# Performance work log

Measured on AMD Instinct MI355X. Metric: run time of the kernel, lower is better.

Reference implementation:

```python
import jax, jax.numpy as jnp
import numpy as np

CAUSAL = True


def setup_inputs() -> dict:
    key = jax.random.key(0)
    k1, k2, k3 = jax.random.split(key, 3)
    B, H, T, D = 2, 16, 2048, 64
    q = jax.random.normal(k1, (B, H, T, D), dtype=jnp.float32)
    k = jax.random.normal(k2, (B, H, T, D), dtype=jnp.float32)
    v = jax.random.normal(k3, (B, H, T, D), dtype=jnp.float32)
    return {"q": q, "k": k, "v": v}


def reference(q, k, v):
    # q,k,v: [B,H,T,D]
    d = q.shape[-1]
    scale = d ** -0.5
    dots = jnp.einsum('bhid,bhjd->bhij', q, k) * scale  # [B,H,T,T]
    if CAUSAL:
        t = q.shape[2]
        mask = jnp.triu(jnp.ones((t, t), dtype=bool), k=1)  # True above diagonal
        dots = jnp.where(mask, -jnp.inf, dots)
    attn = jax.nn.softmax(dots, axis=-1)
    # torch.einsum('bhjd,bhij->bhid', v, attn) == attn @ v
    return jnp.einsum('bhij,bhjd->bhid', attn, v)
```

## Files before the change

### kernel.cpp

```cpp
#include <hip/hip_runtime.h>
#include <hip/hip_bf16.h>

typedef unsigned short u16;
typedef unsigned int u32;
typedef __bf16 bf16x8 __attribute__((ext_vector_type(8)));
typedef u16 u16x8 __attribute__((ext_vector_type(8)));
typedef float floatx4 __attribute__((ext_vector_type(4)));

#define T_SEQ 2048
#define HDIM 64
#define NBH 32

static __device__ __forceinline__ u16 f2b_rne(float x) {
    union { float f; u32 u; } c; c.f = x;
    u32 u = c.u;
    return (u16)((u + 0x7fffu + ((u >> 16) & 1u)) >> 16);
}
static __device__ __forceinline__ u16 f2b_trunc(float x) {
    union { float f; u32 u; } c; c.f = x;
    return (u16)(c.u >> 16);
}

#define GLOAD_LDS16(gp, lp)                                                      \
    __builtin_amdgcn_global_load_lds(                                            \
        (const __attribute__((address_space(1))) u32*)(gp),                      \
        (__attribute__((address_space(3))) u32*)(lp), 16, 0, 0)

#define WAIT_VM(N) asm volatile("s_waitcnt vmcnt(" #N ")" ::: "memory")

__global__ __launch_bounds__(256) void prep(const float* __restrict__ k,
                                            const float* __restrict__ v,
                                            u16* __restrict__ kb,
                                            u16* __restrict__ vt) {
    __shared__ u16 tile[64][68];
    const int bh = blockIdx.y, t0 = blockIdx.x * 64;
    const int tid = threadIdx.x;

    const float* ksrc = k + ((size_t)bh * T_SEQ + t0) * HDIM;
    u16* kdst = kb + ((size_t)bh * T_SEQ + t0) * HDIM;
#pragma unroll
    for (int p = 0; p < 4; p++) {
        int idx = p * 256 + tid;
        float4 f = ((const float4*)ksrc)[idx];
        ushort4 o;
        o.x = f2b_rne(f.x); o.y = f2b_rne(f.y); o.z = f2b_rne(f.z); o.w = f2b_rne(f.w);
        ((ushort4*)kdst)[idx] = o;
    }

    const float* vsrc = v + ((size_t)bh * T_SEQ + t0) * HDIM;
#pragma unroll
    for (int p = 0; p < 4; p++) {
        int idx = p * 256 + tid;
        int r = idx >> 4, c4 = (idx & 15) * 4;
        float4 f = *(const float4*)(vsrc + r * HDIM + c4);
        tile[c4 + 0][r] = f2b_rne(f.x);
        tile[c4 + 1][r] = f2b_rne(f.y);
        tile[c4 + 2][r] = f2b_rne(f.z);
        tile[c4 + 3][r] = f2b_rne(f.w);
    }
    __syncthreads();
    u16* dst = vt + (size_t)bh * HDIM * T_SEQ + t0;
#pragma unroll
    for (int p = 0; p < 2; p++) {
        int idx = p * 256 + tid;
        int d = idx >> 3, pb = idx & 7;
        int k0 = (pb >> 2) * 32 + (pb & 3) * 4;
        union { u16x8 v8; ushort4 q[2]; } w;
        w.q[0] = *(ushort4*)&tile[d][k0];
        w.q[1] = *(ushort4*)&tile[d][k0 + 16];
        *(u16x8*)(dst + (size_t)d * T_SEQ + pb * 8) = w.v8;
    }
}

__global__ __launch_bounds__(512, 4) void fattn(const float* __restrict__ q,
                                                const u16* __restrict__ kb,
                                                const u16* __restrict__ vtb,
                                                float* __restrict__ out) {
    __shared__ __align__(16) u16 Kl[4][64 * 64];
    __shared__ __align__(16) u16 Vl[4][64 * 64];

    const int id = blockIdx.x;
    const int xcd = id & 7;
    const int u = id >> 3;
    const int bh = xcd * 4 + (u & 3);
    const int s = u >> 2;
    const int pr = (s & 8) ? (s ^ 7) : s;
    const int qtHi = 31 - pr, qtLo = pr;

    const int tid = threadIdx.x;
    const int wave = tid >> 6, lane = tid & 63;
    const int l15 = lane & 15, quad = lane >> 4;
    const int tile_sel = wave >> 2;
    const int qhalf = (wave >> 1) & 1;
    const int khalf = wave & 1;
    const int qt = tile_sel ? qtLo : qtHi;
    const int qrow_base = qt * 64 + qhalf * 32;

    const float* qp = q + (size_t)bh * T_SEQ * HDIM;
    const u16* kp = kb + (size_t)bh * T_SEQ * HDIM;
    const u16* vp = vtb + (size_t)bh * HDIM * T_SEQ;

    const int srow = wave * 8 + (lane >> 3);
    const int slot = lane & 7;
    const u16* kg0 = kp + srow * HDIM + (slot ^ (srow & 7)) * 8;
    const u16* vg0 = vp + (size_t)srow * T_SEQ + ((slot - srow) & 7) * 8;

    auto stage = [&](int j, int buf) {
        GLOAD_LDS16(kg0 + j * 64 * HDIM, &Kl[buf][wave * 512]);
        GLOAD_LDS16(vg0 + j * 64, &Vl[buf][wave * 512]);
    };

    const float SL2E = 0.125f * 1.44269504088896f;
    bf16x8 qf[2][2];
    {
#pragma unroll
        for (int qb = 0; qb < 2; qb++) {
            const float* qrow = qp + (size_t)(qrow_base + qb * 16 + l15) * HDIM;
#pragma unroll
            for (int kc = 0; kc < 2; kc++) {
                const float4* p4 = (const float4*)(qrow + kc * 32 + quad * 8);
                float4 fa = p4[0], fb = p4[1];
                union { bf16x8 v; u16 s[8]; } cv;
                cv.s[0] = f2b_rne(fa.x * SL2E); cv.s[1] = f2b_rne(fa.y * SL2E);
                cv.s[2] = f2b_rne(fa.z * SL2E); cv.s[3] = f2b_rne(fa.w * SL2E);
                cv.s[4] = f2b_rne(fb.x * SL2E); cv.s[5] = f2b_rne(fb.y * SL2E);
                cv.s[6] = f2b_rne(fb.z * SL2E); cv.s[7] = f2b_rne(fb.w * SL2E);
                qf[qb][kc] = cv.v;
            }
        }
    }

    union { u16 h[8]; bf16x8 v; } onesu;
#pragma unroll
    for (int i = 0; i < 8; i++) onesu.h[i] = 0x3F80;
    const bf16x8 ones = onesu.v;

    stage(0, 0);
    stage(1, 1);
    stage(2, 2);

    floatx4 o_acc[2][4];
    floatx4 lsacc[2];
#pragma unroll
    for (int qb = 0; qb < 2; qb++) {
        lsacc[qb] = (floatx4){0.f, 0.f, 0.f, 0.f};
#pragma unroll
        for (int dt = 0; dt < 4; dt++) o_acc[qb][dt] = (floatx4){0.f, 0.f, 0.f, 0.f};
    }

    for (int j = 0; j <= qtHi; ++j) {
        if (j + 2 <= qtHi)      WAIT_VM(4);
        else if (j + 1 <= qtHi) WAIT_VM(2);
        else                    WAIT_VM(0);
        __builtin_amdgcn_s_barrier();

        const int cur = j & 3;
        const bool active = (j <= qt);

        bf16x8 kf[2][2];
        if (active) {
            const u16* Kc = Kl[cur];
#pragma unroll
            for (int kc = 0; kc < 2; kc++)
#pragma unroll
                for (int kb2 = 0; kb2 < 2; kb2++) {
                    int rk = khalf * 32 + kb2 * 16 + l15;
                    kf[kc][kb2] = *(const bf16x8*)(Kc + rk * 64 + ((kc * 4 + quad) ^ (rk & 7)) * 8);
                }
        }
        if (j + 3 <= qtHi) stage(j + 3, (j + 3) & 3);
        if (!active) continue;

        floatx4 sacc[2][2];
#pragma unroll
        for (int kb2 = 0; kb2 < 2; kb2++)
#pragma unroll
            for (int qb = 0; qb < 2; qb++) sacc[kb2][qb] = (floatx4){0.f, 0.f, 0.f, 0.f};
        __builtin_amdgcn_s_setprio(1);
#pragma unroll
        for (int kc = 0; kc < 2; kc++)
#pragma unroll
            for (int kb2 = 0; kb2 < 2; kb2++)
#pragma unroll
                for (int qb = 0; qb < 2; qb++)
                    sacc[kb2][qb] = __builtin_amdgcn_mfma_f32_16x16x32_bf16(
                        kf[kc][kb2], qf[qb][kc], sacc[kb2][qb], 0, 0, 0);
        __builtin_amdgcn_s_setprio(0);

        union { bf16x8 v; u16 h[8]; } pk[2];
        if (j == qt) {
            const int key0 = khalf * 32 + quad * 4;
#pragma unroll
            for (int qb = 0; qb < 2; qb++) {
                const int gq = qhalf * 32 + qb * 16 + l15;
#pragma unroll
                for (int kb2 = 0; kb2 < 2; kb2++)
#pragma unroll
                    for (int rg = 0; rg < 4; rg++) {
                        float e = __builtin_amdgcn_exp2f(sacc[kb2][qb][rg]);
                        if (key0 + kb2 * 16 + rg > gq) e = 0.f;
                        pk[qb].h[kb2 * 4 + rg] = f2b_trunc(e);
                    }
            }
        } else {
#pragma unroll
            for (int qb = 0; qb < 2; qb++)
#pragma unroll
                for (int kb2 = 0; kb2 < 2; kb2++)
#pragma unroll
                    for (int rg = 0; rg < 4; rg++)
                        pk[qb].h[kb2 * 4 + rg] =
                            f2b_trunc(__builtin_amdgcn_exp2f(sacc[kb2][qb][rg]));
        }

        const u16* Vc = Vl[cur];
        bf16x8 vf[4];
#pragma unroll
        for (int dt = 0; dt < 4; dt++) {
            int d = dt * 16 + l15;
            vf[dt] = *(const bf16x8*)(Vc + d * 64 + ((khalf * 4 + quad + d) & 7) * 8);
        }

        __builtin_amdgcn_s_setprio(1);
#pragma unroll
        for (int dt = 0; dt < 4; dt++)
#pragma unroll
            for (int qb = 0; qb < 2; qb++)
                o_acc[qb][dt] = __builtin_amdgcn_mfma_f32_16x16x32_bf16(
                    pk[qb].v, vf[dt], o_acc[qb][dt], 0, 0, 0);
        lsacc[0] = __builtin_amdgcn_mfma_f32_16x16x32_bf16(pk[0].v, ones, lsacc[0], 0, 0, 0);
        lsacc[1] = __builtin_amdgcn_mfma_f32_16x16x32_bf16(pk[1].v, ones, lsacc[1], 0, 0, 0);
        __builtin_amdgcn_s_setprio(0);
    }

    __syncthreads();
    const int r = wave >> 1;
    float* xch = ((r & 2) ? (float*)&Vl[0][0] : (float*)&Kl[0][0]) + (r & 1) * 2560;
    floatx4* xv = (floatx4*)xch;
    if (khalf == 0) {
#pragma unroll
        for (int qb = 0; qb < 2; qb++)
#pragma unroll
            for (int dt = 0; dt < 4; dt++) xv[(qb * 4 + dt) * 64 + lane] = o_acc[qb][dt];
        xv[8 * 64 + lane] = lsacc[0];
        xv[9 * 64 + lane] = lsacc[1];
    }
    __syncthreads();
    if (khalf == 1) {
#pragma unroll
        for (int qb = 0; qb < 2; qb++) {
#pragma unroll
            for (int dt = 0; dt < 4; dt++) o_acc[qb][dt] += xv[(qb * 4 + dt) * 64 + lane];
            lsacc[qb] += xv[(8 + qb) * 64 + lane];
        }
        float* op = out + (size_t)bh * T_SEQ * HDIM;
#pragma unroll
        for (int qb = 0; qb < 2; qb++)
#pragma unroll
            for (int rg = 0; rg < 4; rg++) {
                float inv = 1.0f / lsacc[qb][rg];
                size_t row = (size_t)(qrow_base + qb * 16 + quad * 4 + rg) * HDIM;
#pragma unroll
                for (int dt = 0; dt < 4; dt++)
                    op[row + dt * 16 + l15] = o_acc[qb][dt][rg] * inv;
            }
    }
}

extern "C" void kernel_launch(void* const* d_in, const int* in_sizes, int n_in,
                              void* d_out, int out_size, void* d_ws, size_t ws_size,
                              hipStream_t stream) {
    const float* q = (const float*)d_in[0];
    const float* k = (const float*)d_in[1];
    const float* v = (const float*)d_in[2];
    float* out = (float*)d_out;

    u16* kb = (u16*)d_ws;
    u16* vt = kb + (size_t)NBH * T_SEQ * HDIM;

    prep<<<dim3(T_SEQ / 64, NBH), 256, 0, stream>>>(k, v, kb, vt);
    fattn<<<dim3(512), 512, 0, stream>>>(q, kb, vt, out);
}
```

Measured before the change: 119.5 us.

## Replace LDS-staged K/V pipeline with direct global register double-buffering

Removes the shared-memory ring buffer fed by global_load_lds and instead has each wave load its K and V fragments directly from global memory into registers, double-buffered across iterations. Blocks shrink to four waves handling one query tile each, launched heaviest-first instead of pairing heavy and light causal tiles. This eliminates barriers and LDS traffic but duplicates K/V global/L2 reads across waves that previously shared staged tiles, and relies on the scheduler for causal load balance.

```diff
diff --git a/kernel.cpp b/kernel.cpp
--- a/kernel.cpp
+++ b/kernel.cpp
@@ -20,13 +20,6 @@
     union { float f; u32 u; } c; c.f = x;
     return (u16)(c.u >> 16);
 }
-
-#define GLOAD_LDS16(gp, lp)                                                      \
-    __builtin_amdgcn_global_load_lds(                                            \
-        (const __attribute__((address_space(1))) u32*)(gp),                      \
-        (__attribute__((address_space(3))) u32*)(lp), 16, 0, 0)
-
-#define WAIT_VM(N) asm volatile("s_waitcnt vmcnt(" #N ")" ::: "memory")
 
 __global__ __launch_bounds__(256) void prep(const float* __restrict__ k,
                                             const float* __restrict__ v,
@@ -72,61 +65,60 @@
     }
 }
 
-__global__ __launch_bounds__(512, 4) void fattn(const float* __restrict__ q,
+__global__ __launch_bounds__(256, 3) void fattn(const float* __restrict__ q,
                                                 const u16* __restrict__ kb,
                                                 const u16* __restrict__ vtb,
                                                 float* __restrict__ out) {
-    __shared__ __align__(16) u16 Kl[4][64 * 64];
-    __shared__ __align__(16) u16 Vl[4][64 * 64];
+    __shared__ __align__(16) floatx4 xch[2][10][64];
 
     const int id = blockIdx.x;
     const int xcd = id & 7;
-    const int u = id >> 3;
-    const int bh = xcd * 4 + (u & 3);
-    const int s = u >> 2;
-    const int pr = (s & 8) ? (s ^ 7) : s;
-    const int qtHi = 31 - pr, qtLo = pr;
+    const int bh = xcd * 4 + ((id >> 3) & 3);
+    const int qt = 31 - (id >> 5);
 
     const int tid = threadIdx.x;
     const int wave = tid >> 6, lane = tid & 63;
     const int l15 = lane & 15, quad = lane >> 4;
-    const int tile_sel = wave >> 2;
-    const int qhalf = (wave >> 1) & 1;
+    const int qhalf = wave >> 1;
     const int khalf = wave & 1;
-    const int qt = tile_sel ? qtLo : qtHi;
     const int qrow_base = qt * 64 + qhalf * 32;
 
     const float* qp = q + (size_t)bh * T_SEQ * HDIM;
     const u16* kp = kb + (size_t)bh * T_SEQ * HDIM;
     const u16* vp = vtb + (size_t)bh * HDIM * T_SEQ;
 
-    const int srow = wave * 8 + (lane >> 3);
-    const int slot = lane & 7;
-    const u16* kg0 = kp + srow * HDIM + (slot ^ (srow & 7)) * 8;
-    const u16* vg0 = vp + (size_t)srow * T_SEQ + ((slot - srow) & 7) * 8;
-
-    auto stage = [&](int j, int buf) {
-        GLOAD_LDS16(kg0 + j * 64 * HDIM, &Kl[buf][wave * 512]);
-        GLOAD_LDS16(vg0 + j * 64, &Vl[buf][wave * 512]);
+    const u16* kg = kp + (khalf * 32 + l15) * HDIM + quad * 8;
+    const u16* vg = vp + (size_t)l15 * T_SEQ + khalf * 32 + quad * 8;
+
+    bf16x8 kfA[2][2], kfB[2][2], vfA[4], vfB[4];
+    auto load_tiles = [&](int j, bf16x8 (&kf)[2][2], bf16x8 (&vf)[4]) {
+        const u16* kj = kg + j * 64 * HDIM;
+#pragma unroll
+        for (int kc = 0; kc < 2; kc++)
+#pragma unroll
+            for (int kb2 = 0; kb2 < 2; kb2++)
+                kf[kc][kb2] = *(const bf16x8*)(kj + kb2 * 16 * HDIM + kc * 32);
+        const u16* vj = vg + j * 64;
+#pragma unroll
+        for (int dt = 0; dt < 4; dt++)
+            vf[dt] = *(const bf16x8*)(vj + dt * 16 * T_SEQ);
     };
 
     const float SL2E = 0.125f * 1.44269504088896f;
     bf16x8 qf[2][2];
-    {
-#pragma unroll
-        for (int qb = 0; qb < 2; qb++) {
-            const float* qrow = qp + (size_t)(qrow_base + qb * 16 + l15) * HDIM;
-#pragma unroll
-            for (int kc = 0; kc < 2; kc++) {
-                const float4* p4 = (const float4*)(qrow + kc * 32 + quad * 8);
-                float4 fa = p4[0], fb = p4[1];
-                union { bf16x8 v; u16 s[8]; } cv;
-                cv.s[0] = f2b_rne(fa.x * SL2E); cv.s[1] = f2b_rne(fa.y * SL2E);
-                cv.s[2] = f2b_rne(fa.z * SL2E); cv.s[3] = f2b_rne(fa.w * SL2E);
-                cv.s[4] = f2b_rne(fb.x * SL2E); cv.s[5] = f2b_rne(fb.y * SL2E);
-                cv.s[6] = f2b_rne(fb.z * SL2E); cv.s[7] = f2b_rne(fb.w * SL2E);
-                qf[qb][kc] = cv.v;
-            }
+#pragma unroll
+    for (int qb = 0; qb < 2; qb++) {
+        const float* qrow = qp + (size_t)(qrow_base + qb * 16 + l15) * HDIM;
+#pragma unroll
+        for (int kc = 0; kc < 2; kc++) {
+            const float4* p4 = (const float4*)(qrow + kc * 32 + quad * 8);
+            float4 fa = p4[0], fb = p4[1];
+            union { bf16x8 v; u16 s[8]; } cv;
+            cv.s[0] = f2b_rne(fa.x * SL2E); cv.s[1] = f2b_rne(fa.y * SL2E);
+            cv.s[2] = f2b_rne(fa.z * SL2E); cv.s[3] = f2b_rne(fa.w * SL2E);
+            cv.s[4] = f2b_rne(fb.x * SL2E); cv.s[5] = f2b_rne(fb.y * SL2E);
+            cv.s[6] = f2b_rne(fb.z * SL2E); cv.s[7] = f2b_rne(fb.w * SL2E);
+            qf[qb][kc] = cv.v;
         }
     }
 
@@ -135,10 +127,6 @@
     for (int i = 0; i < 8; i++) onesu.h[i] = 0x3F80;
     const bf16x8 ones = onesu.v;
 
-    stage(0, 0);
-    stage(1, 1);
-    stage(2, 2);
-
     floatx4 o_acc[2][4];
     floatx4 lsacc[2];
 #pragma unroll
@@ -148,29 +136,7 @@
         for (int dt = 0; dt < 4; dt++) o_acc[qb][dt] = (floatx4){0.f, 0.f, 0.f, 0.f};
     }
 
-    for (int j = 0; j <= qtHi; ++j) {
-        if (j + 2 <= qtHi)      WAIT_VM(4);
-        else if (j + 1 <= qtHi) WAIT_VM(2);
-        else                    WAIT_VM(0);
-        __builtin_amdgcn_s_barrier();
-
-        const int cur = j & 3;
-        const bool active = (j <= qt);
-
-        bf16x8 kf[2][2];
-        if (active) {
-            const u16* Kc = Kl[cur];
-#pragma unroll
-            for (int kc = 0; kc < 2; kc++)
-#pragma unroll
-                for (int kb2 = 0; kb2 < 2; kb2++) {
-                    int rk = khalf * 32 + kb2 * 16 + l15;
-                    kf[kc][kb2] = *(const bf16x8*)(Kc + rk * 64 + ((kc * 4 + quad) ^ (rk & 7)) * 8);
-                }
-        }
-        if (j + 3 <= qtHi) stage(j + 3, (j + 3) & 3);
-        if (!active) continue;
-
+    auto compute = [&](int j, bf16x8 (&kf)[2][2], bf16x8 (&vf)[4]) {
         floatx4 sacc[2][2];
 #pragma unroll
         for (int kb2 = 0; kb2 < 2; kb2++)
@@ -213,14 +179,6 @@
                             f2b_trunc(__builtin_amdgcn_exp2f(sacc[kb2][qb][rg]));
         }
 
-        const u16* Vc = Vl[cur];
-        bf16x8 vf[4];
-#pragma unroll
-        for (int dt = 0; dt < 4; dt++) {
-            int d = dt * 16 + l15;
-            vf[dt] = *(const bf16x8*)(Vc + d * 64 + ((khalf * 4 + quad + d) & 7) * 8);
-        }
-
         __builtin_amdgcn_s_setprio(1);
 #pragma unroll
         for (int dt = 0; dt < 4; dt++)
@@ -231,31 +189,34 @@
         lsacc[0] = __builtin_amdgcn_mfma_f32_16x16x32_bf16(pk[0].v, ones, lsacc[0], 0, 0, 0);
         lsacc[1] = __builtin_amdgcn_mfma_f32_16x16x32_bf16(pk[1].v, ones, lsacc[1], 0, 0, 0);
         __builtin_amdgcn_s_setprio(0);
-    }
-
-    __syncthreads();
-    const int r = wave >> 1;
-    float* xch = ((r & 2) ? (float*)&Vl[0][0] : (float*)&Kl[0][0]) + (r & 1) * 2560;
-    floatx4* xv = (floatx4*)xch;
+    };
+
+    load_tiles(0, kfA, vfA);
+    for (int j = 0; j <= qt; j += 2) {
+        if (j + 1 <= qt) load_tiles(j + 1, kfB, vfB);
+        compute(j, kfA, vfA);
+        if (j + 1 > qt) break;
+        if (j + 2 <= qt) load_tiles(j + 2, kfA, vfA);
+        compute(j + 1, kfB, vfB);
+    }
+
+    floatx4 (*xv)[64] = xch[qhalf];
     if (khalf == 0) {
 #pragma unroll
         for (int qb = 0; qb < 2; qb++)
 #pragma unroll
-            for (int dt = 0; dt < 4; dt++) xv[(qb * 4 + dt) * 64 + lane] = o_acc[qb][dt];
-        xv[8 * 64 + lane] = lsacc[0];
-        xv[9 * 64 + lane] = lsacc[1];
+            for (int dt = 0; dt < 4; dt++) xv[qb * 4 + dt][lane] = o_acc[qb][dt];
+        xv[8][lane] = lsacc[0];
+        xv[9][lane] = lsacc[1];
     }
     __syncthreads();
     if (khalf == 1) {
+        float* op = out + (size_t)bh * T_SEQ * HDIM;
 #pragma unroll
         for (int qb = 0; qb < 2; qb++) {
 #pragma unroll
-            for (int dt = 0; dt < 4; dt++) o_acc[qb][dt] += xv[(qb * 4 + dt) * 64 + lane];
-            lsacc[qb] += xv[(8 + qb) * 64 + lane];
-        }
-        float* op = out + (size_t)bh * T_SEQ * HDIM;
-#pragma unroll
-        for (int qb = 0; qb < 2; qb++)
+            for (int dt = 0; dt < 4; dt++) o_acc[qb][dt] += xv[qb * 4 + dt][lane];
+            lsacc[qb] += xv[8 + qb][lane];
 #pragma unroll
             for (int rg = 0; rg < 4; rg++) {
                 float inv = 1.0f / lsacc[qb][rg];
@@ -264,6 +225,7 @@
                 for (int dt = 0; dt < 4; dt++)
                     op[row + dt * 16 + l15] = o_acc[qb][dt][rg] * inv;
             }
+        }
     }
 }
 
@@ -279,5 +241,5 @@
     u16* vt = kb + (size_t)NBH * T_SEQ * HDIM;
 
     prep<<<dim3(T_SEQ / 64, NBH), 256, 0, stream>>>(k, v, kb, vt);
-    fattn<<<dim3(512), 512, 0, stream>>>(q, kb, vt, out);
-}
+    fattn<<<dim3(1024), 256, 0, stream>>>(q, kb, vt, out);
+}
```

After: 164.2 us. +37.4%, slower.

## Split long causal query tiles across two blocks with atomic-counter merge

Applied to the files above, without the earlier changes.

Replaces the paired hi/lo query-tile 512-thread blocks with 256-thread blocks. Query tiles 16-31 have their key range split into two chunks handled by separate blocks, which write unnormalized partial outputs and row sums to workspace; the second block to finish, determined by an atomic counter, merges them and normalizes. This aims to balance causal work across 1536 smaller blocks and raise occupancy. The cost is workspace traffic, an atomic and fences, the counter reset in prep, and a shallower double-buffered K/V pipeline with a full barrier each step.

```diff
diff --git a/kernel.cpp b/kernel.cpp
--- a/kernel.cpp
+++ b/kernel.cpp
@@ -26,15 +26,16 @@
         (const __attribute__((address_space(1))) u32*)(gp),                      \
         (__attribute__((address_space(3))) u32*)(lp), 16, 0, 0)
 
-#define WAIT_VM(N) asm volatile("s_waitcnt vmcnt(" #N ")" ::: "memory")
-
 __global__ __launch_bounds__(256) void prep(const float* __restrict__ k,
                                             const float* __restrict__ v,
                                             u16* __restrict__ kb,
-                                            u16* __restrict__ vt) {
+                                            u16* __restrict__ vt,
+                                            u32* __restrict__ cnt) {
     __shared__ u16 tile[64][68];
     const int bh = blockIdx.y, t0 = blockIdx.x * 64;
     const int tid = threadIdx.x;
+
+    if (blockIdx.x == 0 && tid < 16) cnt[bh * 16 + tid] = 0;
 
     const float* ksrc = k + ((size_t)bh * T_SEQ + t0) * HDIM;
     u16* kdst = kb + ((size_t)bh * T_SEQ + t0) * HDIM;
@@ -72,61 +73,73 @@
     }
 }
 
-__global__ __launch_bounds__(512, 4) void fattn(const float* __restrict__ q,
+__global__ __launch_bounds__(256, 4) void fattn(const float* __restrict__ q,
                                                 const u16* __restrict__ kb,
                                                 const u16* __restrict__ vtb,
+                                                float* __restrict__ pws,
+                                                u32* __restrict__ cnt,
                                                 float* __restrict__ out) {
-    __shared__ __align__(16) u16 Kl[4][64 * 64];
-    __shared__ __align__(16) u16 Vl[4][64 * 64];
+    __shared__ __align__(16) u16 Kl[2][64 * 64];
+    __shared__ __align__(16) u16 Vl[2][64 * 64];
+    __shared__ int who;
 
     const int id = blockIdx.x;
-    const int xcd = id & 7;
-    const int u = id >> 3;
-    const int bh = xcd * 4 + (u & 3);
-    const int s = u >> 2;
-    const int pr = (s & 8) ? (s ^ 7) : s;
-    const int qtHi = 31 - pr, qtLo = pr;
+    const int bh = (id & 7) * 4 + ((id >> 3) & 3);
+    const int ks = id >> 5;
+    int qt, j0, j1, ci;
+    bool single;
+    if (ks < 16) {
+        qt = 16 + ks; j0 = 0; j1 = 15; ci = 0; single = false;
+    } else if (((ks - 16) & 1) == 0) {
+        int h = (ks - 16) >> 1;
+        qt = 31 - h; j0 = 16; j1 = qt; ci = 1; single = false;
+    } else {
+        int h = (ks - 16) >> 1;
+        qt = 15 - h; j0 = 0; j1 = qt; ci = 0; single = true;
+    }
 
     const int tid = threadIdx.x;
     const int wave = tid >> 6, lane = tid & 63;
     const int l15 = lane & 15, quad = lane >> 4;
-    const int tile_sel = wave >> 2;
     const int qhalf = (wave >> 1) & 1;
     const int khalf = wave & 1;
-    const int qt = tile_sel ? qtLo : qtHi;
     const int qrow_base = qt * 64 + qhalf * 32;
 
     const float* qp = q + (size_t)bh * T_SEQ * HDIM;
     const u16* kp = kb + (size_t)bh * T_SEQ * HDIM;
     const u16* vp = vtb + (size_t)bh * HDIM * T_SEQ;
 
-    const int srow = wave * 8 + (lane >> 3);
+    const int srow = wave * 16 + (lane >> 3);
     const int slot = lane & 7;
     const u16* kg0 = kp + srow * HDIM + (slot ^ (srow & 7)) * 8;
     const u16* vg0 = vp + (size_t)srow * T_SEQ + ((slot - srow) & 7) * 8;
 
     auto stage = [&](int j, int buf) {
-        GLOAD_LDS16(kg0 + j * 64 * HDIM, &Kl[buf][wave * 512]);
-        GLOAD_LDS16(vg0 + j * 64, &Vl[buf][wave * 512]);
+        const u16* ksrc = kg0 + j * 64 * HDIM;
+        u16* Kd = &Kl[buf][wave * 1024];
+        GLOAD_LDS16(ksrc, Kd);
+        GLOAD_LDS16(ksrc + 8 * HDIM, Kd + 512);
+        const u16* vs2 = vg0 + j * 64;
+        u16* Vd = &Vl[buf][wave * 1024];
+        GLOAD_LDS16(vs2, Vd);
+        GLOAD_LDS16(vs2 + 8 * T_SEQ, Vd + 512);
     };
 
     const float SL2E = 0.125f * 1.44269504088896f;
     bf16x8 qf[2][2];
-    {
-#pragma unroll
-        for (int qb = 0; qb < 2; qb++) {
-            const float* qrow = qp + (size_t)(qrow_base + qb * 16 + l15) * HDIM;
-#pragma unroll
-            for (int kc = 0; kc < 2; kc++) {
-                const float4* p4 = (const float4*)(qrow + kc * 32 + quad * 8);
-                float4 fa = p4[0], fb = p4[1];
-                union { bf16x8 v; u16 s[8]; } cv;
-                cv.s[0] = f2b_rne(fa.x * SL2E); cv.s[1] = f2b_rne(fa.y * SL2E);
-                cv.s[2] = f2b_rne(fa.z * SL2E); cv.s[3] = f2b_rne(fa.w * SL2E);
-                cv.s[4] = f2b_rne(fb.x * SL2E); cv.s[5] = f2b_rne(fb.y * SL2E);
-                cv.s[6] = f2b_rne(fb.z * SL2E); cv.s[7] = f2b_rne(fb.w * SL2E);
-                qf[qb][kc] = cv.v;
-            }
+#pragma unroll
+    for (int qb = 0; qb < 2; qb++) {
+        const float* qrow = qp + (size_t)(qrow_base + qb * 16 + l15) * HDIM;
+#pragma unroll
+        for (int kc = 0; kc < 2; kc++) {
+            const float4* p4 = (const float4*)(qrow + kc * 32 + quad * 8);
+            float4 fa = p4[0], fb = p4[1];
+            union { bf16x8 v; u16 s[8]; } cv;
+            cv.s[0] = f2b_rne(fa.x * SL2E); cv.s[1] = f2b_rne(fa.y * SL2E);
+            cv.s[2] = f2b_rne(fa.z * SL2E); cv.s[3] = f2b_rne(fa.w * SL2E);
+            cv.s[4] = f2b_rne(fb.x * SL2E); cv.s[5] = f2b_rne(fb.y * SL2E);
+            cv.s[6] = f2b_rne(fb.z * SL2E); cv.s[7] = f2b_rne(fb.w * SL2E);
+            qf[qb][kc] = cv.v;
         }
     }
 
@@ -135,9 +148,7 @@
     for (int i = 0; i < 8; i++) onesu.h[i] = 0x3F80;
     const bf16x8 ones = onesu.v;
 
-    stage(0, 0);
-    stage(1, 1);
-    stage(2, 2);
+    stage(j0, 0);
 
     floatx4 o_acc[2][4];
     floatx4 lsacc[2];
@@ -148,29 +159,20 @@
         for (int dt = 0; dt < 4; dt++) o_acc[qb][dt] = (floatx4){0.f, 0.f, 0.f, 0.f};
     }
 
-    for (int j = 0; j <= qtHi; ++j) {
-        if (j + 2 <= qtHi)      WAIT_VM(4);
-        else if (j + 1 <= qtHi) WAIT_VM(2);
-        else                    WAIT_VM(0);
-        __builtin_amdgcn_s_barrier();
-
-        const int cur = j & 3;
-        const bool active = (j <= qt);
+    for (int j = j0; j <= j1; ++j) {
+        __syncthreads();
+        const int cur = (j - j0) & 1;
+        if (j < j1) stage(j + 1, cur ^ 1);
 
         bf16x8 kf[2][2];
-        if (active) {
-            const u16* Kc = Kl[cur];
-#pragma unroll
-            for (int kc = 0; kc < 2; kc++)
-#pragma unroll
-                for (int kb2 = 0; kb2 < 2; kb2++) {
-                    int rk = khalf * 32 + kb2 * 16 + l15;
-                    kf[kc][kb2] = *(const bf16x8*)(Kc + rk * 64 + ((kc * 4 + quad) ^ (rk & 7)) * 8);
-                }
-        }
-        if (j + 3 <= qtHi) stage(j + 3, (j + 3) & 3);
-        if (!active) continue;
-
+        const u16* Kc = Kl[cur];
+#pragma unroll
+        for (int kc = 0; kc < 2; kc++)
+#pragma unroll
+            for (int kb2 = 0; kb2 < 2; kb2++) {
+                int rk = khalf * 32 + kb2 * 16 + l15;
+                kf[kc][kb2] = *(const bf16x8*)(Kc + rk * 64 + ((kc * 4 + quad) ^ (rk & 7)) * 8);
+            }
         floatx4 sacc[2][2];
 #pragma unroll
         for (int kb2 = 0; kb2 < 2; kb2++)
@@ -234,16 +236,14 @@
     }
 
     __syncthreads();
-    const int r = wave >> 1;
-    float* xch = ((r & 2) ? (float*)&Vl[0][0] : (float*)&Kl[0][0]) + (r & 1) * 2560;
-    floatx4* xv = (floatx4*)xch;
+    floatx4* xv = (floatx4*)(qhalf ? (void*)&Vl[0][0] : (void*)&Kl[0][0]);
     if (khalf == 0) {
 #pragma unroll
-        for (int qb = 0; qb < 2; qb++)
+        for (int qb = 0; qb < 2; qb++) {
 #pragma unroll
             for (int dt = 0; dt < 4; dt++) xv[(qb * 4 + dt) * 64 + lane] = o_acc[qb][dt];
-        xv[8 * 64 + lane] = lsacc[0];
-        xv[9 * 64 + lane] = lsacc[1];
+            xv[(8 + qb) * 64 + lane] = lsacc[qb];
+        }
     }
     __syncthreads();
     if (khalf == 1) {
@@ -253,16 +253,61 @@
             for (int dt = 0; dt < 4; dt++) o_acc[qb][dt] += xv[(qb * 4 + dt) * 64 + lane];
             lsacc[qb] += xv[(8 + qb) * 64 + lane];
         }
+    }
+
+    if (single) {
+        if (khalf == 1) {
+            float* op = out + (size_t)bh * T_SEQ * HDIM;
+#pragma unroll
+            for (int qb = 0; qb < 2; qb++)
+#pragma unroll
+                for (int rg = 0; rg < 4; rg++) {
+                    float inv = 1.0f / lsacc[qb][rg];
+                    size_t row = (size_t)(qrow_base + qb * 16 + quad * 4 + rg) * HDIM;
+#pragma unroll
+                    for (int dt = 0; dt < 4; dt++)
+                        op[row + dt * 16 + l15] = o_acc[qb][dt][rg] * inv;
+                }
+        }
+        return;
+    }
+
+    const int tix = bh * 16 + (qt - 16);
+    float* P = pws + (size_t)(tix * 2 + ci) * 4160;
+    if (khalf == 1) {
+#pragma unroll
+        for (int qb = 0; qb < 2; qb++)
+#pragma unroll
+            for (int rg = 0; rg < 4; rg++) {
+                int row = qhalf * 32 + qb * 16 + quad * 4 + rg;
+#pragma unroll
+                for (int dt = 0; dt < 4; dt++)
+                    P[row * 64 + dt * 16 + l15] = o_acc[qb][dt][rg];
+                if (l15 == 0) P[4096 + row] = lsacc[qb][rg];
+            }
+    }
+    __syncthreads();
+    if (tid == 0) {
+        __threadfence();
+        who = atomicAdd(&cnt[tix], 1);
+    }
+    __syncthreads();
+    if (who == 0) return;
+    __threadfence();
+    const float* Po = pws + (size_t)(tix * 2 + (ci ^ 1)) * 4160;
+    if (khalf == 1) {
         float* op = out + (size_t)bh * T_SEQ * HDIM;
 #pragma unroll
         for (int qb = 0; qb < 2; qb++)
 #pragma unroll
             for (int rg = 0; rg < 4; rg++) {
-                float inv = 1.0f / lsacc[qb][rg];
-                size_t row = (size_t)(qrow_base + qb * 16 + quad * 4 + rg) * HDIM;
+                int row = qhalf * 32 + qb * 16 + quad * 4 + rg;
+                float inv = 1.0f / (lsacc[qb][rg] + Po[4096 + row]);
+                size_t orow = (size_t)(qt * 64 + row) * HDIM;
 #pragma unroll
                 for (int dt = 0; dt < 4; dt++)
-                    op[row + dt * 16 + l15] = o_acc[qb][dt][rg] * inv;
+                    op[orow + dt * 16 + l15] =
+                        (o_acc[qb][dt][rg] + Po[row * 64 + dt * 16 + l15]) * inv;
             }
     }
 }
@@ -277,7 +322,9 @@
 
     u16* kb = (u16*)d_ws;
     u16* vt = kb + (size_t)NBH * T_SEQ * HDIM;
-
-    prep<<<dim3(T_SEQ / 64, NBH), 256, 0, stream>>>(k, v, kb, vt);
-    fattn<<<dim3(512), 512, 0, stream>>>(q, kb, vt, out);
-}
+    float* pws = (float*)(vt + (size_t)NBH * T_SEQ * HDIM);
+    u32* cnt = (u32*)(pws + (size_t)1024 * 4160);
+
+    prep<<<dim3(T_SEQ / 64, NBH), 256, 0, stream>>>(k, v, kb, vt, cnt);
+    fattn<<<dim3(1536), 256, 0, stream>>>(q, kb, vt, pws, cnt, out);
+}
```

Result: slower. 230.1 us (+92.6%).
